# Kernel optimization log

Hardware: AMD Instinct MI355X
Metric: run time of the kernel (lower is better)

## Reference

```python
import jax, jax.numpy as jnp
import numpy as np

# Model dims
B, T, D = 1, 2048, 2048          # batch, seq_len, d_model
HI, DI = 4, 64                   # indexer heads / dim
H, DH = 16, 128                  # attention heads / head dim (H*DH == D)
TOPK = 512                       # sparse top-k tokens per query
NEG = -1e9


def setup_inputs() -> dict:
    key = jax.random.key(0)
    ks = jax.random.split(key, 8)
    s = 0.02  # weight init scale
    return {
        "hidden_states": jax.random.normal(ks[0], (B, T, D), jnp.float32),
        "Wq_idx": jax.random.normal(ks[1], (D, HI * DI), jnp.float32) * s,
        "Wk_idx": jax.random.normal(ks[2], (D, DI), jnp.float32) * s,
        "Ww_idx": jax.random.normal(ks[3], (D, HI), jnp.float32) * s,
        "Wq": jax.random.normal(ks[4], (D, H * DH), jnp.float32) * s,
        "Wk": jax.random.normal(ks[5], (D, H * DH), jnp.float32) * s,
        "Wv": jax.random.normal(ks[6], (D, H * DH), jnp.float32) * s,
        "Wo": jax.random.normal(ks[7], (H * DH, D), jnp.float32) * s,
    }


def reference(hidden_states, Wq_idx, Wk_idx, Ww_idx, Wq, Wk, Wv, Wo):
    x = hidden_states
    # ---- Lightning indexer: I[t,s] = sum_j w[t,j] * relu(q[t,j] . k[s]) ----
    qi = (x @ Wq_idx).reshape(B, T, HI, DI)          # [B,T,HI,DI]
    ki = x @ Wk_idx                                   # [B,S,DI]
    w = x @ Ww_idx                                    # [B,T,HI]
    dots = jnp.einsum('bthd,bsd->bths', qi, ki)       # [B,T,HI,S]
    index_scores = (jax.nn.relu(dots) * w[..., None]).sum(axis=2)  # [B,T,S]

    # ---- Top-k token selection with causal mask ----
    causal = jnp.triu(jnp.ones((T, T), dtype=bool), 1)            # True above diag
    masked_scores = jnp.where(causal[None], NEG, index_scores)
    _, top_idx = jax.lax.top_k(masked_scores, TOPK)               # [B,T,TOPK]
    b_ix = jnp.arange(B)[:, None, None]
    t_ix = jnp.arange(T)[None, :, None]
    top_mask = jnp.zeros((B, T, T), dtype=bool).at[b_ix, t_ix, top_idx].set(True)
    add_mask = jnp.where(top_mask, 0.0, NEG).astype(x.dtype)      # [B,T,S]

    # ---- Dense multi-head attention with additive sparse mask ----
    q = (x @ Wq).reshape(B, T, H, DH)
    k = (x @ Wk).reshape(B, T, H, DH)
    v = (x @ Wv).reshape(B, T, H, DH)
    scores = jnp.einsum('bthd,bshd->bhts', q, k) / np.sqrt(DH).astype(np.float32)
    scores = scores + add_mask[:, None]                            # [B,H,T,S]
    probs = jax.nn.softmax(scores, axis=-1)
    attn = jnp.einsum('bhts,bshd->bthd', probs, v).reshape(B, T, H * DH)
    attn_output = attn @ Wo                                        # [B,T,D]
    return attn_output
```

## Files before the change

kernel.cpp:

```cpp
#include <hip/hip_runtime.h>
#include <cstdint>
#include <cstddef>

#define T_DIM 2048
#define D_DIM 2048
#define HI_N 4
#define DI_N 64
#define H_N 16
#define DH_N 128
#define TOPK_N 512
#define NEG_F (-1e9f)
#define FA_NEG (-1e30f)

typedef __attribute__((ext_vector_type(8))) short short8;
typedef __attribute__((ext_vector_type(4))) float f32x4;
typedef unsigned short ushort_t;

__device__ __forceinline__ unsigned short f2bf(float f) {
  unsigned u = __float_as_uint(f);
  u += 0x7FFFu + ((u >> 16) & 1u);
  return (unsigned short)(u >> 16);
}
__device__ __forceinline__ float bf2f(unsigned short b) {
  return __uint_as_float((unsigned)b << 16);
}

__global__ __launch_bounds__(256) void idx_proj(const float* __restrict__ x,
                                                const float* __restrict__ Wq_idx,
                                                const float* __restrict__ Wk_idx,
                                                const float* __restrict__ Ww_idx,
                                                float* __restrict__ qi,
                                                float* __restrict__ ki,
                                                float* __restrict__ wI) {
  __shared__ float As[2][16][64];
  __shared__ float Bs[2][16][64];
  const int bm = blockIdx.y << 6;
  const int bn_id = blockIdx.x;
  const float* B; float* C; int ldB, cb, ncols;
  if (bn_id < 4)       { B = Wq_idx; C = qi; ldB = 256; cb = bn_id << 6; ncols = 64; }
  else if (bn_id == 4) { B = Wk_idx; C = ki; ldB = 64;  cb = 0;          ncols = 64; }
  else                 { B = Ww_idx; C = wI; ldB = 4;   cb = 0;          ncols = 4;  }
  const int tid = threadIdx.x;
  const int tx = tid & 15, ty = tid >> 4;
  const int am = tid >> 2;
  const int ak = (tid & 3) << 2;
  float acc[4][4] = {};

  float4 a4 = *(const float4*)&x[(size_t)(bm + am) * 2048 + ak];
  float4 b4 = make_float4(0, 0, 0, 0);
  if ((tx << 2) < ncols) b4 = *(const float4*)&B[(size_t)ty * ldB + cb + (tx << 2)];
  As[0][ak + 0][am] = a4.x; As[0][ak + 1][am] = a4.y;
  As[0][ak + 2][am] = a4.z; As[0][ak + 3][am] = a4.w;
  *(float4*)&Bs[0][ty][tx << 2] = b4;

  int p = 0;
  for (int k0 = 0; k0 < 2048; k0 += 16) {
    __syncthreads();
    const bool more = (k0 + 16) < 2048;
    if (more) {
      a4 = *(const float4*)&x[(size_t)(bm + am) * 2048 + k0 + 16 + ak];
      if ((tx << 2) < ncols)
        b4 = *(const float4*)&B[(size_t)(k0 + 16 + ty) * ldB + cb + (tx << 2)];
    }
#pragma unroll
    for (int kk = 0; kk < 16; ++kk) {
      float4 av4 = *(const float4*)&As[p][kk][ty << 2];
      float4 bv4 = *(const float4*)&Bs[p][kk][tx << 2];
      float av[4] = {av4.x, av4.y, av4.z, av4.w};
      float bv[4] = {bv4.x, bv4.y, bv4.z, bv4.w};
#pragma unroll
      for (int i = 0; i < 4; ++i)
#pragma unroll
        for (int j = 0; j < 4; ++j) acc[i][j] += av[i] * bv[j];
    }
    if (more) {
      As[1 - p][ak + 0][am] = a4.x; As[1 - p][ak + 1][am] = a4.y;
      As[1 - p][ak + 2][am] = a4.z; As[1 - p][ak + 3][am] = a4.w;
      *(float4*)&Bs[1 - p][ty][tx << 2] = b4;
    }
    p ^= 1;
  }
#pragma unroll
  for (int i = 0; i < 4; ++i) {
    int m = bm + (ty << 2) + i;
    int n0 = tx << 2;
    if (n0 + 3 < ncols) {
      *(float4*)&C[(size_t)m * ldB + cb + n0] =
          make_float4(acc[i][0], acc[i][1], acc[i][2], acc[i][3]);
    } else {
#pragma unroll
      for (int j = 0; j < 4; ++j)
        if (n0 + j < ncols) C[(size_t)m * ldB + cb + n0 + j] = acc[i][j];
    }
  }
}

__global__ __launch_bounds__(256) void cast_bf16(const float* __restrict__ in,
                                                 ushort_t* __restrict__ out) {
  int i = (blockIdx.x * 256 + threadIdx.x) * 4;
  float4 f = *(const float4*)(in + i);
  ushort4 o;
  o.x = f2bf(f.x); o.y = f2bf(f.y); o.z = f2bf(f.z); o.w = f2bf(f.w);
  *(ushort4*)(out + i) = o;
}

__global__ __launch_bounds__(256) void cast_transpose(const float* __restrict__ in,
                                                      ushort_t* __restrict__ out,
                                                      int R, int C) {
  __shared__ float tile[32][33];
  const int bx = blockIdx.x * 32;
  const int by = blockIdx.y * 32;
  const int tx = threadIdx.x & 31, ty = threadIdx.x >> 5;
#pragma unroll
  for (int i = 0; i < 32; i += 8)
    tile[ty + i][tx] = in[(size_t)(by + ty + i) * C + bx + tx];
  __syncthreads();
#pragma unroll
  for (int i = 0; i < 32; i += 8)
    out[(size_t)(bx + ty + i) * R + by + tx] = f2bf(tile[tx][ty + i]);
}

__global__ __launch_bounds__(256) void transpose_bf(const ushort_t* __restrict__ in,
                                                    ushort_t* __restrict__ out,
                                                    int ldin) {
  __shared__ ushort_t tile[64][68];
  const int bx = blockIdx.x * 64;
  const int by = blockIdx.y * 64;
  const int tid = threadIdx.x;
#pragma unroll
  for (int p = 0; p < 4; ++p) {
    int r = p * 16 + (tid >> 4), c0 = (tid & 15) * 4;
    *(ushort4*)&tile[r][c0] = *(const ushort4*)(in + (size_t)(by + r) * ldin + bx + c0);
  }
  __syncthreads();
#pragma unroll
  for (int p = 0; p < 4; ++p) {
    int r = p * 16 + (tid >> 4), c0 = (tid & 15) * 4;
    ushort4 o;
    o.x = tile[c0 + 0][r]; o.y = tile[c0 + 1][r];
    o.z = tile[c0 + 2][r]; o.w = tile[c0 + 3][r];
    *(ushort4*)(out + (size_t)(bx + r) * T_DIM + by + c0) = o;
  }
}

template <int OUT_BF16>
__global__ __launch_bounds__(256) void gemm_bt(const ushort_t* __restrict__ A,
                                               const ushort_t* __restrict__ Bt,
                                               void* __restrict__ C,
                                               int M, int N, int K) {
  __shared__ __attribute__((aligned(16))) ushort_t As[128 * 64];
  __shared__ __attribute__((aligned(16))) ushort_t Bs[128 * 64];
  const int bm = blockIdx.y << 7;
  const int bn = blockIdx.x << 7;
  const int tid = threadIdx.x;
  const int lane = tid & 63;
  const int wv = tid >> 6;
  const int wm = (wv >> 1) << 6;
  const int wn = (wv & 1) << 6;

  f32x4 acc[4][4] = {};

  const int sr = tid >> 3;
  const int sc = (tid & 7) << 3;
  const ushort_t* ga = A + (size_t)(bm + sr) * K + sc;
  const ushort_t* gb = Bt + (size_t)(bn + sr) * K + sc;
  const size_t rstep = (size_t)32 * K;

  for (int k0 = 0; k0 < K; k0 += 64) {
#pragma unroll
    for (int i = 0; i < 4; ++i) {
      __builtin_amdgcn_global_load_lds(
          (const __attribute__((address_space(1))) unsigned int*)(ga + i * rstep + k0),
          (__attribute__((address_space(3))) unsigned int*)(As + i * 2048 + tid * 8),
          16, 0, 0);
      __builtin_amdgcn_global_load_lds(
          (const __attribute__((address_space(1))) unsigned int*)(gb + i * rstep + k0),
          (__attribute__((address_space(3))) unsigned int*)(Bs + i * 2048 + tid * 8),
          16, 0, 0);
    }
    __syncthreads();
#pragma unroll
    for (int ks = 0; ks < 2; ++ks) {
      short8 af[4], bfr[4];
      const int kk = (ks << 5) + ((lane >> 4) << 3);
#pragma unroll
      for (int i = 0; i < 4; ++i) {
        af[i]  = *(const short8*)(As + (wm + (i << 4) + (lane & 15)) * 64 + kk);
        bfr[i] = *(const short8*)(Bs + (wn + (i << 4) + (lane & 15)) * 64 + kk);
      }
#pragma unroll
      for (int i = 0; i < 4; ++i)
#pragma unroll
        for (int j = 0; j < 4; ++j)
          acc[i][j] = __builtin_amdgcn_mfma_f32_16x16x32_bf16(af[i], bfr[j], acc[i][j], 0, 0, 0);
    }
    __syncthreads();
  }

  const int lrow = (lane >> 4) << 2;
  const int lcol = lane & 15;
#pragma unroll
  for (int i = 0; i < 4; ++i) {
    const int row = bm + wm + (i << 4) + lrow;
#pragma unroll
    for (int j = 0; j < 4; ++j) {
      const int col = bn + wn + (j << 4) + lcol;
#pragma unroll
      for (int r = 0; r < 4; ++r) {
        if (OUT_BF16)
          ((ushort_t*)C)[(size_t)(row + r) * N + col] = f2bf(acc[i][j][r]);
        else
          ((float*)C)[(size_t)(row + r) * N + col] = acc[i][j][r];
      }
    }
  }
}

__global__ __launch_bounds__(256) void idx_scores_rt(const float* __restrict__ qi,
                                                     const float* __restrict__ ki,
                                                     const float* __restrict__ w,
                                                     float* __restrict__ out) {
  const int t0 = blockIdx.y << 6, s0 = blockIdx.x << 6;
  const int tid = threadIdx.x;
  const int tx = tid & 15, ty = tid >> 4;
  if (s0 > t0 + 63) {
    const float4 nf = make_float4(NEG_F, NEG_F, NEG_F, NEG_F);
#pragma unroll
    for (int i = 0; i < 4; ++i) {
      int m = t0 + (ty << 2) + i;
      *(float4*)&out[(size_t)m * T_DIM + s0 + (tx << 2)] = nf;
    }
    return;
  }
  __shared__ float As[16][64];
  __shared__ float Bs[16][64];
  __shared__ float wsh[64][4];
  if (tid < 64) *(float4*)wsh[tid] = *(const float4*)&w[(size_t)(t0 + tid) * 4];
  const int am = tid >> 2;
  const int ak = (tid & 3) << 2;
  float oacc[4][4] = {};
#pragma unroll
  for (int h = 0; h < HI_N; ++h) {
    float dacc[4][4] = {};
    for (int k0 = 0; k0 < DI_N; k0 += 16) {
      float4 qa = *(const float4*)&qi[(size_t)(t0 + am) * 256 + h * DI_N + k0 + ak];
      float4 kb = *(const float4*)&ki[(size_t)(s0 + am) * DI_N + k0 + ak];
      __syncthreads();
      As[ak + 0][am] = qa.x; As[ak + 1][am] = qa.y;
      As[ak + 2][am] = qa.z; As[ak + 3][am] = qa.w;
      Bs[ak + 0][am] = kb.x; Bs[ak + 1][am] = kb.y;
      Bs[ak + 2][am] = kb.z; Bs[ak + 3][am] = kb.w;
      __syncthreads();
#pragma unroll
      for (int kk = 0; kk < 16; ++kk) {
        float4 a4 = *(const float4*)&As[kk][ty << 2];
        float4 b4 = *(const float4*)&Bs[kk][tx << 2];
        float av[4] = {a4.x, a4.y, a4.z, a4.w};
        float bv[4] = {b4.x, b4.y, b4.z, b4.w};
#pragma unroll
        for (int i = 0; i < 4; ++i)
#pragma unroll
          for (int j = 0; j < 4; ++j) dacc[i][j] += av[i] * bv[j];
      }
    }
#pragma unroll
    for (int i = 0; i < 4; ++i) {
      float wh = wsh[(ty << 2) + i][h];
#pragma unroll
      for (int j = 0; j < 4; ++j) oacc[i][j] += fmaxf(dacc[i][j], 0.f) * wh;
    }
  }
#pragma unroll
  for (int i = 0; i < 4; ++i) {
    int m = t0 + (ty << 2) + i;
    int n0 = s0 + (tx << 2);
    float4 r;
    r.x = (n0 + 0 > m) ? NEG_F : oacc[i][0];
    r.y = (n0 + 1 > m) ? NEG_F : oacc[i][1];
    r.z = (n0 + 2 > m) ? NEG_F : oacc[i][2];
    r.w = (n0 + 3 > m) ? NEG_F : oacc[i][3];
    *(float4*)&out[(size_t)m * T_DIM + n0] = r;
  }
}

__global__ __launch_bounds__(256) void select_mask(const float* __restrict__ scores,
                                                   unsigned long long* __restrict__ maskbits) {
  const int t = blockIdx.x, tid = threadIdx.x;
  __shared__ unsigned int hist[256];
  __shared__ unsigned int s_prefix, s_krem;
  __shared__ unsigned char bytes[256];
  unsigned int uv[8];
  const float* row = scores + (size_t)t * T_DIM;
  {
    float4 f0 = *(const float4*)(row + tid * 8);
    float4 f1 = *(const float4*)(row + tid * 8 + 4);
    float fv[8] = {f0.x, f0.y, f0.z, f0.w, f1.x, f1.y, f1.z, f1.w};
#pragma unroll
    for (int j = 0; j < 8; ++j) {
      unsigned u = __float_as_uint(fv[j]);
      uv[j] = (u & 0x80000000u) ? ~u : (u | 0x80000000u);
    }
  }
  if (tid == 0) { s_prefix = 0u; s_krem = TOPK_N; }
  for (int p = 0; p < 4; ++p) {
    const int sh = 24 - 8 * p;
    hist[tid] = 0;
    __syncthreads();
    const unsigned pm = p ? (0xFFFFFFFFu << (32 - 8 * p)) : 0u;
    const unsigned prefix = s_prefix;
#pragma unroll
    for (int j = 0; j < 8; ++j)
      if ((uv[j] & pm) == prefix) atomicAdd(&hist[(uv[j] >> sh) & 255], 1u);
    __syncthreads();
    if (tid == 0) {
      unsigned krem = s_krem, cum = 0;
      int b = 255;
      for (;; --b) { cum += hist[b]; if (cum >= krem) break; }
      s_prefix = prefix | ((unsigned)b << sh);
      s_krem = krem - (cum - hist[b]);
    }
    __syncthreads();
  }
  const unsigned V = s_prefix;
  const int kr = (int)s_krem;
  int eqc = 0;
#pragma unroll
  for (int j = 0; j < 8; ++j) eqc += (uv[j] == V);
  __syncthreads();
  hist[tid] = (unsigned)eqc;
  __syncthreads();
  for (int off = 1; off < 256; off <<= 1) {
    int v = (int)hist[tid];
    if (tid >= off) v += (int)hist[tid - off];
    __syncthreads();
    hist[tid] = (unsigned)v;
    __syncthreads();
  }
  int run = (int)hist[tid] - eqc;
  unsigned char byte = 0;
#pragma unroll
  for (int j = 0; j < 8; ++j) {
    bool eq = (uv[j] == V);
    bool take = (uv[j] > V) || (eq && run < kr);
    run += eq;
    byte |= (unsigned char)(take ? (1u << j) : 0u);
  }
  bytes[tid] = byte;
  __syncthreads();
  if (tid < 32) {
    unsigned long long wqw = 0;
#pragma unroll
    for (int b = 0; b < 8; ++b)
      wqw |= (unsigned long long)bytes[tid * 8 + b] << (8 * b);
    maskbits[(size_t)t * 32 + tid] = wqw;
  }
}

__global__ __launch_bounds__(256, 1) void flash_attn(
    const ushort_t* __restrict__ q, const ushort_t* __restrict__ k,
    const ushort_t* __restrict__ vt, const unsigned long long* __restrict__ maskbits,
    ushort_t* __restrict__ attn, int ldqk) {
  __shared__ __attribute__((aligned(16))) ushort_t Ks[2][128 * 128];
  __shared__ __attribute__((aligned(16))) ushort_t Vts[128 * 128];
  __shared__ __attribute__((aligned(16))) ushort_t Ps[128 * 136];
  __shared__ float mstate[2][128], lstate[2][128];
  __shared__ float pmax[2][128], psum[2][128];

  const int tt = blockIdx.x;
  const int h  = blockIdx.y;
  const int t0 = tt << 7;
  const int tid = threadIdx.x;
  const int lane = tid & 63;
  const int wv = tid >> 6;
  const int wm = (wv >> 1) << 6;
  const int wn = (wv & 1) << 6;
  const int l15 = lane & 15, l4 = lane >> 4;
  const int e3 = l15 & 7;
  const int scol = (((tid & 15) ^ ((tid >> 4) & 7)) << 3);

  if (tid < 128) { mstate[0][tid] = -INFINITY; lstate[0][tid] = 0.f; }

  {
    const ushort_t* gq = q + (size_t)(t0 + (tid >> 4)) * ldqk + h * DH_N + scol;
#pragma unroll
    for (int p = 0; p < 8; ++p)
      __builtin_amdgcn_global_load_lds(
          (const __attribute__((address_space(1))) unsigned int*)(gq + (size_t)p * 16 * ldqk),
          (__attribute__((address_space(3))) unsigned int*)(Ks[0] + p * 2048 + tid * 8), 16, 0, 0);
  }
  asm volatile("s_waitcnt vmcnt(0)" ::: "memory");
  __builtin_amdgcn_s_barrier();
  asm volatile("" ::: "memory");
  short8 qfrag[4][4];
#pragma unroll
  for (int ks = 0; ks < 4; ++ks)
#pragma unroll
    for (int i = 0; i < 4; ++i)
      qfrag[ks][i] = *(const short8*)(Ks[0] + (wm + i * 16 + l15) * 128 +
                                      ((((ks << 2) + l4) ^ e3) << 3));
  asm volatile("s_waitcnt lgkmcnt(0)" ::: "memory");
  __builtin_amdgcn_s_barrier();
  asm volatile("" ::: "memory");

  f32x4 acc[4][4] = {};
  const int nst = (tt < 4) ? 4 : (tt + 1);
  const bool owner = ((wv & 1) == 0) && (l15 == 0);
  const float rsc = 0.08838834764831845f;

  {
    const ushort_t* gk = k + (size_t)(tid >> 4) * ldqk + h * DH_N + scol;
#pragma unroll
    for (int p = 0; p < 8; ++p)
      __builtin_amdgcn_global_load_lds(
          (const __attribute__((address_space(1))) unsigned int*)(gk + (size_t)p * 16 * ldqk),
          (__attribute__((address_space(3))) unsigned int*)(Ks[0] + p * 2048 + tid * 8), 16, 0, 0);
  }

  for (int st = 0; st < nst; ++st) {
    const int s0 = st << 7;
    const bool pf = (st + 1) < nst;

    asm volatile("" ::: "memory");
    __builtin_amdgcn_s_barrier();
    asm volatile("" ::: "memory");

    unsigned long long mw[4][4];
    {
      const int wbase = (s0 >> 6) + (wn >> 6);
#pragma unroll
      for (int i = 0; i < 4; ++i)
#pragma unroll
        for (int r = 0; r < 4; ++r)
          mw[i][r] = maskbits[(size_t)(t0 + wm + i * 16 + l4 * 4 + r) * 32 + wbase];
    }
    {
      const ushort_t* gv = vt + (size_t)(h * DH_N + (tid >> 4)) * T_DIM + s0 + scol;
#pragma unroll
      for (int p = 0; p < 8; ++p)
        __builtin_amdgcn_global_load_lds(
            (const __attribute__((address_space(1))) unsigned int*)(gv + (size_t)p * 16 * T_DIM),
            (__attribute__((address_space(3))) unsigned int*)(Vts + p * 2048 + tid * 8), 16, 0, 0);
    }
    asm volatile("" ::: "memory");
    if (pf) {
      const ushort_t* gk = k + (size_t)(s0 + 128 + (tid >> 4)) * ldqk + h * DH_N + scol;
      ushort_t* dst = Ks[(st + 1) & 1];
#pragma unroll
      for (int p = 0; p < 8; ++p)
        __builtin_amdgcn_global_load_lds(
            (const __attribute__((address_space(1))) unsigned int*)(gk + (size_t)p * 16 * ldqk),
            (__attribute__((address_space(3))) unsigned int*)(dst + p * 2048 + tid * 8), 16, 0, 0);
    }
    if (pf) asm volatile("s_waitcnt vmcnt(32)" ::: "memory");
    else    asm volatile("s_waitcnt vmcnt(24)" ::: "memory");
    __builtin_amdgcn_s_barrier();
    asm volatile("" ::: "memory");

    const ushort_t* Kb = Ks[st & 1];
    f32x4 sacc[4][4] = {};
    __builtin_amdgcn_s_setprio(1);
#pragma unroll
    for (int ks = 0; ks < 4; ++ks) {
      short8 bfr[4];
      const int co = ((((ks << 2) + l4) ^ e3) << 3);
#pragma unroll
      for (int j = 0; j < 4; ++j)
        bfr[j] = *(const short8*)(Kb + (wn + j * 16 + l15) * 128 + co);
#pragma unroll
      for (int i = 0; i < 4; ++i)
#pragma unroll
        for (int j = 0; j < 4; ++j)
          sacc[i][j] = __builtin_amdgcn_mfma_f32_16x16x32_bf16(qfrag[ks][i], bfr[j], sacc[i][j], 0, 0, 0);
    }
    __builtin_amdgcn_s_setprio(0);

#pragma unroll
    for (int i = 0; i < 4; ++i)
#pragma unroll
      for (int j = 0; j < 4; ++j)
#pragma unroll
        for (int r = 0; r < 4; ++r) {
          bool sel = (mw[i][r] >> (j * 16 + l15)) & 1;
          sacc[i][j][r] = sel ? sacc[i][j][r] * rsc : FA_NEG;
        }
    float pmx[4][4];
#pragma unroll
    for (int i = 0; i < 4; ++i)
#pragma unroll
      for (int r = 0; r < 4; ++r) {
        float m0 = fmaxf(fmaxf(sacc[i][0][r], sacc[i][1][r]), fmaxf(sacc[i][2][r], sacc[i][3][r]));
#pragma unroll
        for (int off = 1; off < 16; off <<= 1) m0 = fmaxf(m0, __shfl_xor(m0, off));
        pmx[i][r] = m0;
      }
    if (l15 == 0)
#pragma unroll
      for (int i = 0; i < 4; ++i)
#pragma unroll
        for (int r = 0; r < 4; ++r)
          pmax[wv & 1][wm + i * 16 + l4 * 4 + r] = pmx[i][r];
    asm volatile("s_waitcnt lgkmcnt(0)" ::: "memory");
    __builtin_amdgcn_s_barrier();
    asm volatile("" ::: "memory");

    const int rp = st & 1, wp = 1 - rp;
    float nmr[4][4];
#pragma unroll
    for (int i = 0; i < 4; ++i)
#pragma unroll
      for (int r = 0; r < 4; ++r) {
        int rw = wm + i * 16 + l4 * 4 + r;
        nmr[i][r] = fmaxf(mstate[rp][rw], fmaxf(pmax[0][rw], pmax[1][rw]));
      }
    float alpha_c[4];
#pragma unroll
    for (int j = 0; j < 4; ++j) {
      int col = wn + j * 16 + l15;
      float mo = mstate[rp][col];
      float nc = fmaxf(mo, fmaxf(pmax[0][col], pmax[1][col]));
      alpha_c[j] = __expf(mo - nc);
    }
    if (owner)
#pragma unroll
      for (int i = 0; i < 4; ++i)
#pragma unroll
        for (int r = 0; r < 4; ++r)
          mstate[wp][wm + i * 16 + l4 * 4 + r] = nmr[i][r];

    float psr[4][4] = {};
#pragma unroll
    for (int i = 0; i < 4; ++i)
#pragma unroll
      for (int j = 0; j < 4; ++j)
#pragma unroll
        for (int r = 0; r < 4; ++r) {
          float s = sacc[i][j][r];
          float pv = (s <= -1e29f) ? 0.f : __expf(s - nmr[i][r]);
          sacc[i][j][r] = pv;
          psr[i][r] += pv;
        }
#pragma unroll
    for (int i = 0; i < 4; ++i)
#pragma unroll
      for (int j = 0; j < 4; ++j) {
        int col = wn + j * 16 + l15;
#pragma unroll
        for (int r = 0; r < 4; ++r)
          Ps[(wm + i * 16 + l4 * 4 + r) * 136 + col] = f2bf(sacc[i][j][r]);
      }
#pragma unroll
    for (int i = 0; i < 4; ++i)
#pragma unroll
      for (int r = 0; r < 4; ++r) {
        float sv = psr[i][r];
#pragma unroll
        for (int off = 1; off < 16; off <<= 1) sv += __shfl_xor(sv, off);
        psr[i][r] = sv;
      }
    if (l15 == 0)
#pragma unroll
      for (int i = 0; i < 4; ++i)
#pragma unroll
        for (int r = 0; r < 4; ++r)
          psum[wv & 1][wm + i * 16 + l4 * 4 + r] = psr[i][r];
#pragma unroll
    for (int i = 0; i < 4; ++i)
#pragma unroll
      for (int j = 0; j < 4; ++j)
#pragma unroll
        for (int r = 0; r < 4; ++r)
          acc[i][j][r] *= alpha_c[j];

    asm volatile("s_waitcnt lgkmcnt(0)" ::: "memory");
    if (pf) asm volatile("s_waitcnt vmcnt(8)" ::: "memory");
    else    asm volatile("s_waitcnt vmcnt(0)" ::: "memory");
    __builtin_amdgcn_s_barrier();
    asm volatile("" ::: "memory");

    if (owner)
#pragma unroll
      for (int i = 0; i < 4; ++i)
#pragma unroll
        for (int r = 0; r < 4; ++r) {
          int rw = wm + i * 16 + l4 * 4 + r;
          float al = __expf(mstate[rp][rw] - nmr[i][r]);
          lstate[wp][rw] = al * lstate[rp][rw] + psum[0][rw] + psum[1][rw];
        }
    __builtin_amdgcn_s_setprio(1);
#pragma unroll
    for (int ks = 0; ks < 4; ++ks) {
      short8 af[4], bfr[4];
      const int co = ((((ks << 2) + l4) ^ e3) << 3);
#pragma unroll
      for (int i = 0; i < 4; ++i)
        af[i] = *(const short8*)(Vts + (wm + i * 16 + l15) * 128 + co);
#pragma unroll
      for (int j = 0; j < 4; ++j)
        bfr[j] = *(const short8*)(Ps + (wn + j * 16 + l15) * 136 + ks * 32 + l4 * 8);
#pragma unroll
      for (int i = 0; i < 4; ++i)
#pragma unroll
        for (int j = 0; j < 4; ++j)
          acc[i][j] = __builtin_amdgcn_mfma_f32_16x16x32_bf16(af[i], bfr[j], acc[i][j], 0, 0, 0);
    }
    __builtin_amdgcn_s_setprio(0);
  }
  __syncthreads();
  const int fp = nst & 1;
  float linv[4];
#pragma unroll
  for (int j = 0; j < 4; ++j) linv[j] = 1.f / lstate[fp][wn + j * 16 + l15];
#pragma unroll
  for (int i = 0; i < 4; ++i)
#pragma unroll
    for (int j = 0; j < 4; ++j) {
      int col = wn + j * 16 + l15;
      int dbase = wm + i * 16 + l4 * 4;
      ushort4 pk;
      pk.x = f2bf(acc[i][j][0] * linv[j]);
      pk.y = f2bf(acc[i][j][1] * linv[j]);
      pk.z = f2bf(acc[i][j][2] * linv[j]);
      pk.w = f2bf(acc[i][j][3] * linv[j]);
      *(ushort4*)(Ps + col * 136 + dbase) = pk;
    }
  __syncthreads();
#pragma unroll
  for (int p = 0; p < 8; ++p) {
    int rw = p * 16 + (tid >> 4);
    int d0 = (tid & 15) * 8;
    *(ulonglong2*)(attn + (size_t)(t0 + rw) * D_DIM + h * DH_N + d0) =
        *(const ulonglong2*)(Ps + rw * 136 + d0);
  }
}

extern "C" void kernel_launch(void* const* d_in, const int* in_sizes, int n_in,
                              void* d_out, int out_size, void* d_ws, size_t ws_size,
                              hipStream_t stream) {
  (void)in_sizes; (void)n_in; (void)out_size; (void)ws_size;
  const float* x      = (const float*)d_in[0];
  const float* Wq_idx = (const float*)d_in[1];
  const float* Wk_idx = (const float*)d_in[2];
  const float* Ww_idx = (const float*)d_in[3];
  const float* Wq     = (const float*)d_in[4];
  const float* Wk     = (const float*)d_in[5];
  const float* Wv     = (const float*)d_in[6];
  const float* Wo     = (const float*)d_in[7];
  float* out = (float*)d_out;

  char* ws = (char*)d_ws;
  const size_t MB = 1ull << 20;
  float*    scores  = (float*)(ws);
  ushort_t* qkv_bf  = (ushort_t*)(ws);
  unsigned long long* maskbits = (unsigned long long*)(ws + 25 * MB + 512 * 1024);
  ushort_t* x_bf    = (ushort_t*)(ws + 26 * MB);
  ushort_t* Wcat_t  = (ushort_t*)(ws + 34 * MB);
  ushort_t* vt_bf   = (ushort_t*)(ws + 34 * MB);
  ushort_t* attn_bf = (ushort_t*)(ws + 42 * MB);
  ushort_t* Wo_t    = (ushort_t*)(ws + 58 * MB);
  float*    qi      = (float*)(ws + 66 * MB);
  float*    ki      = (float*)(ws + 68 * MB);
  float*    wI      = (float*)(ws + 68 * MB + 512 * 1024);

  const dim3 blk(256);
  const dim3 tgrid(D_DIM / 32, D_DIM / 32);

  cast_bf16<<<dim3((D_DIM * T_DIM) / 1024), blk, 0, stream>>>(x, x_bf);
  cast_transpose<<<tgrid, blk, 0, stream>>>(Wq, Wcat_t, D_DIM, D_DIM);
  cast_transpose<<<tgrid, blk, 0, stream>>>(Wk, Wcat_t + (size_t)D_DIM * D_DIM, D_DIM, D_DIM);
  cast_transpose<<<tgrid, blk, 0, stream>>>(Wv, Wcat_t + (size_t)2 * D_DIM * D_DIM, D_DIM, D_DIM);
  cast_transpose<<<tgrid, blk, 0, stream>>>(Wo, Wo_t, D_DIM, D_DIM);

  idx_proj<<<dim3(6, T_DIM / 64), blk, 0, stream>>>(x, Wq_idx, Wk_idx, Ww_idx, qi, ki, wI);
  idx_scores_rt<<<dim3(T_DIM / 64, T_DIM / 64), blk, 0, stream>>>(qi, ki, wI, scores);
  select_mask<<<dim3(T_DIM), blk, 0, stream>>>(scores, maskbits);

  gemm_bt<1><<<dim3(3 * D_DIM / 128, T_DIM / 128), blk, 0, stream>>>(
      x_bf, Wcat_t, qkv_bf, T_DIM, 3 * D_DIM, D_DIM);

  transpose_bf<<<dim3(D_DIM / 64, T_DIM / 64), blk, 0, stream>>>(
      qkv_bf + 2 * D_DIM, vt_bf, 3 * D_DIM);

  flash_attn<<<dim3(T_DIM / 128, H_N), blk, 0, stream>>>(
      qkv_bf, qkv_bf + D_DIM, vt_bf, maskbits, attn_bf, 3 * D_DIM);

  gemm_bt<0><<<dim3(D_DIM / 128, T_DIM / 128), blk, 0, stream>>>(
      attn_bf, Wo_t, out, T_DIM, D_DIM, D_DIM);
}
```

Baseline: 586.2 us.

## Give each wave full query rows so softmax state stays in registers

Repartitions flash attention work so each of the four waves owns 32 query rows across all 128 keys, computing S^T with K as the A operand. Row max and sum now need only intra-wave shuffles across the 4 lane groups, and the running max and sum live in registers. This removes the shared-memory pmax/psum/mstate/lstate exchange and one block barrier per key tile. In exchange, K and V fragments are reloaded per wave (8 A-fragments instead of 4), which raises LDS read traffic per wave. Accumulator register footprint is unchanged.

```diff
diff --git a/kernel.cpp b/kernel.cpp
--- a/kernel.cpp
+++ b/kernel.cpp
@@ -363,8 +363,6 @@
   __shared__ __attribute__((aligned(16))) ushort_t Ks[2][128 * 128];
   __shared__ __attribute__((aligned(16))) ushort_t Vts[128 * 128];
   __shared__ __attribute__((aligned(16))) ushort_t Ps[128 * 136];
-  __shared__ float mstate[2][128], lstate[2][128];
-  __shared__ float pmax[2][128], psum[2][128];
 
   const int tt = blockIdx.x;
   const int h  = blockIdx.y;
@@ -372,13 +370,9 @@
   const int tid = threadIdx.x;
   const int lane = tid & 63;
   const int wv = tid >> 6;
-  const int wm = (wv >> 1) << 6;
-  const int wn = (wv & 1) << 6;
   const int l15 = lane & 15, l4 = lane >> 4;
   const int e3 = l15 & 7;
   const int scol = (((tid & 15) ^ ((tid >> 4) & 7)) << 3);
-
-  if (tid < 128) { mstate[0][tid] = -INFINITY; lstate[0][tid] = 0.f; }
 
   {
     const ushort_t* gq = q + (size_t)(t0 + (tid >> 4)) * ldqk + h * DH_N + scol;
@@ -391,20 +385,21 @@
   asm volatile("s_waitcnt vmcnt(0)" ::: "memory");
   __builtin_amdgcn_s_barrier();
   asm volatile("" ::: "memory");
-  short8 qfrag[4][4];
+  short8 qfrag[4][2];
 #pragma unroll
   for (int ks = 0; ks < 4; ++ks)
 #pragma unroll
-    for (int i = 0; i < 4; ++i)
-      qfrag[ks][i] = *(const short8*)(Ks[0] + (wm + i * 16 + l15) * 128 +
+    for (int j = 0; j < 2; ++j)
+      qfrag[ks][j] = *(const short8*)(Ks[0] + (wv * 32 + j * 16 + l15) * 128 +
                                       ((((ks << 2) + l4) ^ e3) << 3));
   asm volatile("s_waitcnt lgkmcnt(0)" ::: "memory");
   __builtin_amdgcn_s_barrier();
   asm volatile("" ::: "memory");
 
-  f32x4 acc[4][4] = {};
+  f32x4 acc[8][2] = {};
+  float m_reg[2] = {-INFINITY, -INFINITY};
+  float l_reg[2] = {0.f, 0.f};
   const int nst = (tt < 4) ? 4 : (tt + 1);
-  const bool owner = ((wv & 1) == 0) && (l15 == 0);
   const float rsc = 0.08838834764831845f;
 
   {
@@ -424,14 +419,14 @@
     __builtin_amdgcn_s_barrier();
     asm volatile("" ::: "memory");
 
-    unsigned long long mw[4][4];
+    unsigned long long mw[2][2];
     {
-      const int wbase = (s0 >> 6) + (wn >> 6);
-#pragma unroll
-      for (int i = 0; i < 4; ++i)
-#pragma unroll
-        for (int r = 0; r < 4; ++r)
-          mw[i][r] = maskbits[(size_t)(t0 + wm + i * 16 + l4 * 4 + r) * 32 + wbase];
+      const int wbase = s0 >> 6;
+#pragma unroll
+      for (int j = 0; j < 2; ++j)
+#pragma unroll
+        for (int wd = 0; wd < 2; ++wd)
+          mw[j][wd] = maskbits[(size_t)(t0 + wv * 32 + j * 16 + l15) * 32 + wbase + wd];
     }
     {
       const ushort_t* gv = vt + (size_t)(h * DH_N + (tid >> 4)) * T_DIM + s0 + scol;
@@ -451,177 +446,121 @@
             (const __attribute__((address_space(1))) unsigned int*)(gk + (size_t)p * 16 * ldqk),
             (__attribute__((address_space(3))) unsigned int*)(dst + p * 2048 + tid * 8), 16, 0, 0);
     }
-    if (pf) asm volatile("s_waitcnt vmcnt(32)" ::: "memory");
-    else    asm volatile("s_waitcnt vmcnt(24)" ::: "memory");
+    if (pf) asm volatile("s_waitcnt vmcnt(20)" ::: "memory");
+    else    asm volatile("s_waitcnt vmcnt(12)" ::: "memory");
     __builtin_amdgcn_s_barrier();
     asm volatile("" ::: "memory");
 
     const ushort_t* Kb = Ks[st & 1];
-    f32x4 sacc[4][4] = {};
+    f32x4 sacc[8][2] = {};
     __builtin_amdgcn_s_setprio(1);
 #pragma unroll
     for (int ks = 0; ks < 4; ++ks) {
-      short8 bfr[4];
       const int co = ((((ks << 2) + l4) ^ e3) << 3);
-#pragma unroll
-      for (int j = 0; j < 4; ++j)
-        bfr[j] = *(const short8*)(Kb + (wn + j * 16 + l15) * 128 + co);
-#pragma unroll
-      for (int i = 0; i < 4; ++i)
-#pragma unroll
-        for (int j = 0; j < 4; ++j)
-          sacc[i][j] = __builtin_amdgcn_mfma_f32_16x16x32_bf16(qfrag[ks][i], bfr[j], sacc[i][j], 0, 0, 0);
+      short8 af[8];
+#pragma unroll
+      for (int i = 0; i < 8; ++i)
+        af[i] = *(const short8*)(Kb + (i * 16 + l15) * 128 + co);
+#pragma unroll
+      for (int i = 0; i < 8; ++i)
+#pragma unroll
+        for (int j = 0; j < 2; ++j)
+          sacc[i][j] = __builtin_amdgcn_mfma_f32_16x16x32_bf16(af[i], qfrag[ks][j], sacc[i][j], 0, 0, 0);
     }
     __builtin_amdgcn_s_setprio(0);
 
 #pragma unroll
-    for (int i = 0; i < 4; ++i)
-#pragma unroll
-      for (int j = 0; j < 4; ++j)
+    for (int i = 0; i < 8; ++i)
+#pragma unroll
+      for (int j = 0; j < 2; ++j)
 #pragma unroll
         for (int r = 0; r < 4; ++r) {
-          bool sel = (mw[i][r] >> (j * 16 + l15)) & 1;
+          bool sel = (mw[j][i >> 2] >> ((i & 3) * 16 + l4 * 4 + r)) & 1;
           sacc[i][j][r] = sel ? sacc[i][j][r] * rsc : FA_NEG;
         }
-    float pmx[4][4];
-#pragma unroll
-    for (int i = 0; i < 4; ++i)
-#pragma unroll
-      for (int r = 0; r < 4; ++r) {
-        float m0 = fmaxf(fmaxf(sacc[i][0][r], sacc[i][1][r]), fmaxf(sacc[i][2][r], sacc[i][3][r]));
-#pragma unroll
-        for (int off = 1; off < 16; off <<= 1) m0 = fmaxf(m0, __shfl_xor(m0, off));
-        pmx[i][r] = m0;
-      }
-    if (l15 == 0)
-#pragma unroll
-      for (int i = 0; i < 4; ++i)
-#pragma unroll
-        for (int r = 0; r < 4; ++r)
-          pmax[wv & 1][wm + i * 16 + l4 * 4 + r] = pmx[i][r];
-    asm volatile("s_waitcnt lgkmcnt(0)" ::: "memory");
-    __builtin_amdgcn_s_barrier();
-    asm volatile("" ::: "memory");
-
-    const int rp = st & 1, wp = 1 - rp;
-    float nmr[4][4];
-#pragma unroll
-    for (int i = 0; i < 4; ++i)
-#pragma unroll
-      for (int r = 0; r < 4; ++r) {
-        int rw = wm + i * 16 + l4 * 4 + r;
-        nmr[i][r] = fmaxf(mstate[rp][rw], fmaxf(pmax[0][rw], pmax[1][rw]));
-      }
-    float alpha_c[4];
-#pragma unroll
-    for (int j = 0; j < 4; ++j) {
-      int col = wn + j * 16 + l15;
-      float mo = mstate[rp][col];
-      float nc = fmaxf(mo, fmaxf(pmax[0][col], pmax[1][col]));
-      alpha_c[j] = __expf(mo - nc);
-    }
-    if (owner)
-#pragma unroll
-      for (int i = 0; i < 4; ++i)
-#pragma unroll
-        for (int r = 0; r < 4; ++r)
-          mstate[wp][wm + i * 16 + l4 * 4 + r] = nmr[i][r];
-
-    float psr[4][4] = {};
-#pragma unroll
-    for (int i = 0; i < 4; ++i)
-#pragma unroll
-      for (int j = 0; j < 4; ++j)
+
+    float alpha[2];
+#pragma unroll
+    for (int j = 0; j < 2; ++j) {
+      float pm = sacc[0][j][0];
+#pragma unroll
+      for (int i = 0; i < 8; ++i)
+#pragma unroll
+        for (int r = 0; r < 4; ++r) pm = fmaxf(pm, sacc[i][j][r]);
+      pm = fmaxf(pm, __shfl_xor(pm, 16));
+      pm = fmaxf(pm, __shfl_xor(pm, 32));
+      const float mn = fmaxf(m_reg[j], pm);
+      alpha[j] = __expf(m_reg[j] - mn);
+      float ps = 0.f;
+#pragma unroll
+      for (int i = 0; i < 8; ++i)
 #pragma unroll
         for (int r = 0; r < 4; ++r) {
           float s = sacc[i][j][r];
-          float pv = (s <= -1e29f) ? 0.f : __expf(s - nmr[i][r]);
+          float pv = (s <= -1e29f) ? 0.f : __expf(s - mn);
           sacc[i][j][r] = pv;
-          psr[i][r] += pv;
+          ps += pv;
         }
-#pragma unroll
-    for (int i = 0; i < 4; ++i)
-#pragma unroll
-      for (int j = 0; j < 4; ++j) {
-        int col = wn + j * 16 + l15;
-#pragma unroll
-        for (int r = 0; r < 4; ++r)
-          Ps[(wm + i * 16 + l4 * 4 + r) * 136 + col] = f2bf(sacc[i][j][r]);
+      ps += __shfl_xor(ps, 16);
+      ps += __shfl_xor(ps, 32);
+      l_reg[j] = alpha[j] * l_reg[j] + ps;
+      m_reg[j] = mn;
+    }
+#pragma unroll
+    for (int i = 0; i < 8; ++i)
+#pragma unroll
+      for (int j = 0; j < 2; ++j)
+#pragma unroll
+        for (int r = 0; r < 4; ++r) acc[i][j][r] *= alpha[j];
+
+#pragma unroll
+    for (int j = 0; j < 2; ++j)
+#pragma unroll
+      for (int i = 0; i < 8; ++i) {
+        ushort4 pk;
+        pk.x = f2bf(sacc[i][j][0]); pk.y = f2bf(sacc[i][j][1]);
+        pk.z = f2bf(sacc[i][j][2]); pk.w = f2bf(sacc[i][j][3]);
+        *(ushort4*)&Ps[(wv * 32 + j * 16 + l15) * 136 + i * 16 + l4 * 4] = pk;
       }
-#pragma unroll
-    for (int i = 0; i < 4; ++i)
-#pragma unroll
-      for (int r = 0; r < 4; ++r) {
-        float sv = psr[i][r];
-#pragma unroll
-        for (int off = 1; off < 16; off <<= 1) sv += __shfl_xor(sv, off);
-        psr[i][r] = sv;
-      }
-    if (l15 == 0)
-#pragma unroll
-      for (int i = 0; i < 4; ++i)
-#pragma unroll
-        for (int r = 0; r < 4; ++r)
-          psum[wv & 1][wm + i * 16 + l4 * 4 + r] = psr[i][r];
-#pragma unroll
-    for (int i = 0; i < 4; ++i)
-#pragma unroll
-      for (int j = 0; j < 4; ++j)
-#pragma unroll
-        for (int r = 0; r < 4; ++r)
-          acc[i][j][r] *= alpha_c[j];
-
-    asm volatile("s_waitcnt lgkmcnt(0)" ::: "memory");
+
     if (pf) asm volatile("s_waitcnt vmcnt(8)" ::: "memory");
     else    asm volatile("s_waitcnt vmcnt(0)" ::: "memory");
     __builtin_amdgcn_s_barrier();
     asm volatile("" ::: "memory");
 
-    if (owner)
-#pragma unroll
-      for (int i = 0; i < 4; ++i)
-#pragma unroll
-        for (int r = 0; r < 4; ++r) {
-          int rw = wm + i * 16 + l4 * 4 + r;
-          float al = __expf(mstate[rp][rw] - nmr[i][r]);
-          lstate[wp][rw] = al * lstate[rp][rw] + psum[0][rw] + psum[1][rw];
-        }
     __builtin_amdgcn_s_setprio(1);
 #pragma unroll
     for (int ks = 0; ks < 4; ++ks) {
-      short8 af[4], bfr[4];
       const int co = ((((ks << 2) + l4) ^ e3) << 3);
-#pragma unroll
-      for (int i = 0; i < 4; ++i)
-        af[i] = *(const short8*)(Vts + (wm + i * 16 + l15) * 128 + co);
-#pragma unroll
-      for (int j = 0; j < 4; ++j)
-        bfr[j] = *(const short8*)(Ps + (wn + j * 16 + l15) * 136 + ks * 32 + l4 * 8);
-#pragma unroll
-      for (int i = 0; i < 4; ++i)
-#pragma unroll
-        for (int j = 0; j < 4; ++j)
-          acc[i][j] = __builtin_amdgcn_mfma_f32_16x16x32_bf16(af[i], bfr[j], acc[i][j], 0, 0, 0);
+      short8 af[8], bq[2];
+#pragma unroll
+      for (int i = 0; i < 8; ++i)
+        af[i] = *(const short8*)(Vts + (i * 16 + l15) * 128 + co);
+#pragma unroll
+      for (int j = 0; j < 2; ++j)
+        bq[j] = *(const short8*)(Ps + (wv * 32 + j * 16 + l15) * 136 + ks * 32 + l4 * 8);
+#pragma unroll
+      for (int i = 0; i < 8; ++i)
+#pragma unroll
+        for (int j = 0; j < 2; ++j)
+          acc[i][j] = __builtin_amdgcn_mfma_f32_16x16x32_bf16(af[i], bq[j], acc[i][j], 0, 0, 0);
     }
     __builtin_amdgcn_s_setprio(0);
   }
-  __syncthreads();
-  const int fp = nst & 1;
-  float linv[4];
-#pragma unroll
-  for (int j = 0; j < 4; ++j) linv[j] = 1.f / lstate[fp][wn + j * 16 + l15];
-#pragma unroll
-  for (int i = 0; i < 4; ++i)
-#pragma unroll
-    for (int j = 0; j < 4; ++j) {
-      int col = wn + j * 16 + l15;
-      int dbase = wm + i * 16 + l4 * 4;
+
+  float linv[2];
+#pragma unroll
+  for (int j = 0; j < 2; ++j) linv[j] = 1.f / l_reg[j];
+#pragma unroll
+  for (int j = 0; j < 2; ++j)
+#pragma unroll
+    for (int i = 0; i < 8; ++i) {
       ushort4 pk;
       pk.x = f2bf(acc[i][j][0] * linv[j]);
       pk.y = f2bf(acc[i][j][1] * linv[j]);
       pk.z = f2bf(acc[i][j][2] * linv[j]);
       pk.w = f2bf(acc[i][j][3] * linv[j]);
-      *(ushort4*)(Ps + col * 136 + dbase) = pk;
+      *(ushort4*)&Ps[(wv * 32 + j * 16 + l15) * 136 + i * 16 + l4 * 4] = pk;
     }
   __syncthreads();
 #pragma unroll
```

After: 545.3 us. -7.0%, faster.
